# Kernel optimization log

Hardware: AMD Instinct MI355X
Metric: run time of the kernel (lower is better)

The kernel has to match this reference:

```python
import jax, jax.numpy as jnp
import numpy as np

N_NODES = 50000
N_EDGES = 1600000
HIDDEN = 1024
NUM_CLASSES = 64


def setup_inputs() -> dict:
    key = jax.random.key(0)
    k1, k2, k3 = jax.random.split(key, 3)
    x = jax.random.normal(k1, (N_NODES, HIDDEN), dtype=jnp.float32)
    edge_index = jax.random.randint(k2, (2, N_EDGES), 0, N_NODES, dtype=jnp.int64)
    # Glorot-style init for the GCNConv linear weight, zero bias (PyG defaults)
    W = jax.random.normal(k3, (HIDDEN, NUM_CLASSES), dtype=jnp.float32) / np.sqrt(HIDDEN)
    b = jnp.zeros((NUM_CLASSES,), dtype=jnp.float32)
    return {"x": x, "edge_index": edge_index, "W": W, "b": b}


def reference(x, edge_index, W, b):
    # GCNConv: add self-loops, symmetric deg^{-1/2} normalization,
    # linear transform, gather-scale-scatter aggregation, bias, then softmax.
    n = x.shape[0]
    loops = jnp.arange(n, dtype=edge_index.dtype)
    src = jnp.concatenate([edge_index[0], loops])  # [E+N]
    dst = jnp.concatenate([edge_index[1], loops])  # [E+N]

    ones = jnp.ones(dst.shape[0], dtype=x.dtype)
    deg = jax.ops.segment_sum(ones, dst, num_segments=n)  # in-degree incl. self-loop
    deg_inv_sqrt = jnp.where(deg > 0, jax.lax.rsqrt(deg), 0.0)
    norm = deg_inv_sqrt[src] * deg_inv_sqrt[dst]  # [E+N]

    h = x @ W  # [N, C] dense GEMM (transform before propagate)
    msgs = h[src] * norm[:, None]  # gather + scale
    out = jax.ops.segment_sum(msgs, dst, num_segments=n) + b  # scatter-add
    return jax.nn.softmax(out, axis=1)
```

## Files before the change

kernel.cpp:

```cpp
#include <hip/hip_runtime.h>
#include <hip/hip_bf16.h>
#include <hip/hip_fp16.h>
#include <math.h>

#define HIDDEN 1024
#define NCLS 64
#define NB2 784
#define BCAP2 2560
#define CHUNK 4096
#define SMEM_BYTES 33280

typedef __attribute__((ext_vector_type(8))) short short8;
typedef __attribute__((ext_vector_type(4))) float f32x4;
typedef __attribute__((ext_vector_type(8))) _Float16 half8;

__device__ __forceinline__ short f2bf(float f) {
    __hip_bfloat16 b = __float2bfloat16(f);
    return __builtin_bit_cast(short, b);
}
__device__ __forceinline__ float bf2f(short s) {
    unsigned u = ((unsigned)(unsigned short)s) << 16;
    return __builtin_bit_cast(float, u);
}

__device__ __forceinline__ void async_copy16(void* lds, const void* g) {
    __builtin_amdgcn_global_load_lds(
        (const __attribute__((address_space(1))) unsigned int*)g,
        (__attribute__((address_space(3))) unsigned int*)lds, 16, 0, 0);
}

__global__ void wprep_kernel(const float* __restrict__ W,
                             short* __restrict__ wt_hi, short* __restrict__ wt_lo) {
    int idx = blockIdx.x * 256 + threadIdx.x;
    int c = idx >> 10;
    int k = idx & 1023;
    float f = W[(size_t)k * NCLS + c];
    short hb = f2bf(f);
    wt_hi[idx] = hb;
    wt_lo[idx] = f2bf(f - bf2f(hb));
}

__device__ void bucket_body(char* smem, const int* __restrict__ ei,
                            unsigned* __restrict__ pairs2, int* __restrict__ bcnt2,
                            int E, int bid) {
    int* hist  = (int*)smem;
    int* offs  = hist + 1024;
    int* cur   = offs + 1024;
    int* gbase = cur + 1024;
    unsigned* stage = (unsigned*)(gbase + 1024);
    int* nz = (int*)(stage + CHUNK);
    int* wsum = nz + 1;

    const int tid = threadIdx.x;
    const int base = bid * CHUNK;
    const int cnt_c = min(CHUNK, E - base);

    if (tid == 0) *nz = 0;
    #pragma unroll
    for (int j = 0; j < 4; ++j) { hist[tid + 256 * j] = 0; cur[tid + 256 * j] = 0; }
    __syncthreads();

    int found = 0;
    for (int j = tid; j < 1024; j += 256) {
        int e = base + j;
        if (e < E) found |= (ei[2 * e + 1] != 0);
    }
    if (found) atomicOr(nz, 1);
    __syncthreads();
    const int is64 = (*nz == 0);

    unsigned pr[16];
    #pragma unroll
    for (int j = 0; j < 16; ++j) {
        int e = base + j * 256 + tid;
        unsigned p = 0xFFFFFFFFu;
        if (e < E) {
            int s = is64 ? ei[2 * e] : ei[e];
            int d = is64 ? ei[2 * (E + e)] : ei[E + e];
            p = (unsigned)s | ((unsigned)d << 16);
            atomicAdd(&hist[d >> 6], 1);
        }
        pr[j] = p;
    }
    __syncthreads();

    const int b0 = 4 * tid;
    int h0 = hist[b0], h1 = hist[b0 + 1], h2 = hist[b0 + 2], h3 = hist[b0 + 3];
    int S = h0 + h1 + h2 + h3;
    int incl = S;
    #pragma unroll
    for (int d = 1; d < 64; d <<= 1) {
        int t2 = __shfl_up(incl, d);
        if ((tid & 63) >= d) incl += t2;
    }
    if ((tid & 63) == 63) wsum[tid >> 6] = incl;
    __syncthreads();
    int pre = 0;
    #pragma unroll
    for (int w = 0; w < 4; ++w)
        if (w < (tid >> 6)) pre += wsum[w];
    int ex = pre + incl - S;
    offs[b0] = ex;
    offs[b0 + 1] = ex + h0;
    offs[b0 + 2] = ex + h0 + h1;
    offs[b0 + 3] = ex + h0 + h1 + h2;
    if (h0 > 0) gbase[b0] = atomicAdd(&bcnt2[b0], h0);
    if (h1 > 0) gbase[b0 + 1] = atomicAdd(&bcnt2[b0 + 1], h1);
    if (h2 > 0) gbase[b0 + 2] = atomicAdd(&bcnt2[b0 + 2], h2);
    if (h3 > 0) gbase[b0 + 3] = atomicAdd(&bcnt2[b0 + 3], h3);
    __syncthreads();

    #pragma unroll
    for (int j = 0; j < 16; ++j) {
        unsigned p = pr[j];
        if (p != 0xFFFFFFFFu) {
            int b = (int)(p >> 22);
            int pos = offs[b] + atomicAdd(&cur[b], 1);
            stage[pos] = p;
        }
    }
    __syncthreads();
    for (int i = tid; i < cnt_c; i += 256) {
        unsigned p = stage[i];
        int b = (int)(p >> 22);
        pairs2[(size_t)b * BCAP2 + gbase[b] + (i - offs[b])] = p;
    }
}

__device__ void gemm_body(char* smem, const float* __restrict__ x,
                          const short* __restrict__ wt_hi, const short* __restrict__ wt_lo,
                          _Float16* __restrict__ h16, int M, int bid) {
    char* As = smem;
    char* Bh = smem + 16 * 1040;
    char* Bl = smem + 24 * 1040;

    const int tid = threadIdx.x;
    const int wave = tid >> 6;
    const int lane = tid & 63;
    const int l15 = lane & 15, l4 = lane >> 4;
    const int row0 = bid * 64;

    const float* agp[4];
    #pragma unroll
    for (int i = 0; i < 4; ++i) {
        int rg = row0 + (wave * 4 + i) * 4 + (lane >> 4);
        if (rg > M - 1) rg = M - 1;
        int g = (lane & 15) ^ (((lane >> 4) & 3) << 2);
        agp[i] = x + (size_t)rg * HIDDEN + g * 4;
    }
    const short* bhp[2];
    const short* blp[2];
    #pragma unroll
    for (int i = 0; i < 2; ++i) {
        int c = (wave * 2 + i) * 8 + (lane >> 3);
        int g = (lane & 7) ^ ((lane >> 3) & 7);
        bhp[i] = wt_hi + (size_t)c * HIDDEN + g * 8;
        blp[i] = wt_lo + (size_t)c * HIDDEN + g * 8;
    }

    f32x4 acc[4];
    #pragma unroll
    for (int nf = 0; nf < 4; ++nf) acc[nf] = (f32x4){0.f, 0.f, 0.f, 0.f};

    const int rt = wave * 16 + l15;
    const int r3 = rt & 3;
    char* arow = As + (rt >> 2) * 1040 + r3 * 256;

    for (int k0 = 0; k0 < HIDDEN; k0 += 64) {
        #pragma unroll
        for (int i = 0; i < 4; ++i)
            async_copy16(As + (wave * 4 + i) * 1040, agp[i] + k0);
        #pragma unroll
        for (int i = 0; i < 2; ++i) {
            async_copy16(Bh + (wave * 2 + i) * 1040, bhp[i] + k0);
            async_copy16(Bl + (wave * 2 + i) * 1040, blp[i] + k0);
        }
        __syncthreads();

        #pragma unroll
        for (int kk = 0; kk < 2; ++kk) {
            int js = (kk * 8 + l4 * 2) ^ (r3 << 2);
            f32x4 af0 = *reinterpret_cast<const f32x4*>(arow + js * 16);
            f32x4 af1 = *reinterpret_cast<const f32x4*>(arow + js * 16 + 16);
            short8 ah, al;
            #pragma unroll
            for (int j = 0; j < 4; ++j) {
                short hb = f2bf(af0[j]);
                ah[j] = hb;
                al[j] = f2bf(af0[j] - bf2f(hb));
                short hb2 = f2bf(af1[j]);
                ah[j + 4] = hb2;
                al[j + 4] = f2bf(af1[j] - bf2f(hb2));
            }
            #pragma unroll
            for (int nf = 0; nf < 4; ++nf) {
                int c = l15 + 16 * nf;
                int jb = (kk * 4 + l4) ^ (c & 7);
                size_t boff = (size_t)(c >> 3) * 1040 + (c & 7) * 128 + jb * 16;
                short8 bh = *reinterpret_cast<const short8*>(Bh + boff);
                short8 bl = *reinterpret_cast<const short8*>(Bl + boff);
                acc[nf] = __builtin_amdgcn_mfma_f32_16x16x32_bf16(ah, bh, acc[nf], 0, 0, 0);
                acc[nf] = __builtin_amdgcn_mfma_f32_16x16x32_bf16(al, bh, acc[nf], 0, 0, 0);
                acc[nf] = __builtin_amdgcn_mfma_f32_16x16x32_bf16(ah, bl, acc[nf], 0, 0, 0);
            }
        }
        __syncthreads();
    }

    #pragma unroll
    for (int j = 0; j < 4; ++j) {
        int r = row0 + wave * 16 + l4 * 4 + j;
        if (r < M) {
            #pragma unroll
            for (int nf = 0; nf < 4; ++nf) {
                h16[(size_t)r * NCLS + l15 + 16 * nf] = (_Float16)acc[nf][j];
            }
        }
    }
}

__global__ __launch_bounds__(256) void fat_kernel(const float* __restrict__ x,
                                                  const short* __restrict__ wt_hi,
                                                  const short* __restrict__ wt_lo,
                                                  _Float16* __restrict__ h16, int M,
                                                  const int* __restrict__ ei,
                                                  unsigned* __restrict__ pairs2,
                                                  int* __restrict__ bcnt2, int E,
                                                  int nGemmGrid, int nTiles) {
    __shared__ __align__(16) char smem[SMEM_BYTES];
    const int bid = blockIdx.x;
    if (bid < nGemmGrid) {
        for (int t = bid; t < nTiles; t += nGemmGrid)
            gemm_body(smem, x, wt_hi, wt_lo, h16, M, t);
    } else {
        bucket_body(smem, ei, pairs2, bcnt2, E, bid - nGemmGrid);
    }
}

__global__ __launch_bounds__(256) void degree_kernel(const unsigned* __restrict__ pairs2,
                                                     const int* __restrict__ bcnt2,
                                                     float* __restrict__ dis, int n) {
    __shared__ int hist[256];
    const int tid = threadIdx.x;
    hist[tid] = 0;
    __syncthreads();
    #pragma unroll
    for (int gg = 0; gg < 4; ++gg) {
        int g = blockIdx.x * 4 + gg;
        const int cb = bcnt2[g];
        const unsigned* bp = pairs2 + (size_t)g * BCAP2;
        for (int i = tid; i < cb; i += 256)
            atomicAdd(&hist[gg * 64 + ((bp[i] >> 16) & 63)], 1);
    }
    __syncthreads();
    int node = blockIdx.x * 256 + tid;
    if (node < n) dis[node] = rsqrtf((float)hist[tid] + 1.0f);
}

__global__ __launch_bounds__(256) void agg_kernel(const unsigned* __restrict__ pairs2,
                                                  const int* __restrict__ bcnt2,
                                                  const _Float16* __restrict__ h16,
                                                  const float* __restrict__ dis,
                                                  const float* __restrict__ bias,
                                                  float* __restrict__ out, int n) {
    __shared__ int hist[64];
    __shared__ int offs[64];
    __shared__ int cur[64];
    __shared__ unsigned short ssrc[BCAP2];
    __shared__ float swt[BCAP2];
    const int tid = threadIdx.x;
    const int grp = blockIdx.x;
    const int base_node = grp * 64;
    if (base_node >= n) return;
    if (tid < 64) { hist[tid] = 0; cur[tid] = 0; }
    __syncthreads();
    const int cb = bcnt2[grp];
    const unsigned* bp = pairs2 + (size_t)grp * BCAP2;
    for (int i = tid; i < cb; i += 256)
        atomicAdd(&hist[(bp[i] >> 16) & 63], 1);
    __syncthreads();
    if (tid == 0) {
        int r = 0;
        #pragma unroll
        for (int k = 0; k < 64; ++k) { offs[k] = r; r += hist[k]; }
    }
    __syncthreads();
    for (int i = tid; i < cb; i += 256) {
        unsigned p = bp[i];
        int ln = (p >> 16) & 63;
        int pos = offs[ln] + atomicAdd(&cur[ln], 1);
        int s = (int)(p & 0xFFFFu);
        ssrc[pos] = (unsigned short)s;
        swt[pos] = dis[s];
    }
    __syncthreads();

    const int wave = tid >> 6;
    const int lane = tid & 63;
    const int q = lane & 7;
    const int g = lane >> 3;
    float bv[8];
    #pragma unroll
    for (int c = 0; c < 8; ++c) bv[c] = bias[q * 8 + c];

    for (int t = 0; t < 16; ++t) {
        int ln = wave * 16 + t;
        int node = base_node + ln;
        if (node >= n) continue;
        int len = hist[ln];
        int e0 = offs[ln];
        float di = rsqrtf((float)len + 1.0f);

        half8 hs = *reinterpret_cast<const half8*>(h16 + (size_t)node * NCLS + q * 8);
        float selfw = (g == 0) ? di : 0.f;
        float a[8], a2[8];
        #pragma unroll
        for (int c = 0; c < 8; ++c) { a[c] = (float)hs[c] * selfw; a2[c] = 0.f; }

        for (int i = 0; i < len; i += 16) {
            int i1 = i + g;
            bool v1 = i1 < len;
            int s1 = v1 ? (int)ssrc[e0 + i1] : 0;
            float w1 = v1 ? swt[e0 + i1] : 0.f;
            half8 r1 = *reinterpret_cast<const half8*>(h16 + (size_t)s1 * NCLS + q * 8);
            if (i + 8 < len) {
                int i2 = i + 8 + g;
                bool v2 = i2 < len;
                int s2 = v2 ? (int)ssrc[e0 + i2] : 0;
                float w2 = v2 ? swt[e0 + i2] : 0.f;
                half8 r2 = *reinterpret_cast<const half8*>(h16 + (size_t)s2 * NCLS + q * 8);
                #pragma unroll
                for (int c = 0; c < 8; ++c) a2[c] += w2 * (float)r2[c];
            }
            #pragma unroll
            for (int c = 0; c < 8; ++c) a[c] += w1 * (float)r1[c];
        }
        #pragma unroll
        for (int c = 0; c < 8; ++c) {
            float s = a[c] + a2[c];
            s += __shfl_xor(s, 8);
            s += __shfl_xor(s, 16);
            s += __shfl_xor(s, 32);
            a[c] = s * di + bv[c];
        }
        float m = a[0];
        #pragma unroll
        for (int c = 1; c < 8; ++c) m = fmaxf(m, a[c]);
        #pragma unroll
        for (int d = 1; d < 8; d <<= 1) m = fmaxf(m, __shfl_xor(m, d));
        float ex[8], sum = 0.f;
        #pragma unroll
        for (int c = 0; c < 8; ++c) { ex[c] = __expf(a[c] - m); sum += ex[c]; }
        #pragma unroll
        for (int d = 1; d < 8; d <<= 1) sum += __shfl_xor(sum, d);
        float inv = 1.f / sum;
        if (g == 0) {
            f32x4 o0 = {ex[0] * inv, ex[1] * inv, ex[2] * inv, ex[3] * inv};
            f32x4 o1 = {ex[4] * inv, ex[5] * inv, ex[6] * inv, ex[7] * inv};
            *reinterpret_cast<f32x4*>(out + (size_t)node * NCLS + q * 8) = o0;
            *reinterpret_cast<f32x4*>(out + (size_t)node * NCLS + q * 8 + 4) = o1;
        }
    }
}

extern "C" void kernel_launch(void* const* d_in, const int* in_sizes, int n_in,
                              void* d_out, int out_size, void* d_ws, size_t ws_size,
                              hipStream_t stream) {
    const float* x    = (const float*)d_in[0];
    const int*   ei   = (const int*)d_in[1];
    const float* W    = (const float*)d_in[2];
    const float* bias = (const float*)d_in[3];
    float* out = (float*)d_out;

    const int n = in_sizes[0] / HIDDEN;
    const int E = in_sizes[1] / 2;

    char* ws = (char*)d_ws;
    size_t off = 0;
    auto alloc = [&](size_t bytes) -> void* {
        void* p = (void*)(ws + off);
        off = (off + bytes + 255) & ~((size_t)255);
        return p;
    };
    int*      bcnt2  = (int*)alloc((size_t)NB2 * 4);
    unsigned* pairs2 = (unsigned*)alloc((size_t)NB2 * BCAP2 * 4);
    float*    dis    = (float*)alloc((size_t)n * 4);
    _Float16* h16    = (_Float16*)alloc((size_t)n * NCLS * 2);
    short*    wt_hi  = (short*)alloc((size_t)NCLS * HIDDEN * 2);
    short*    wt_lo  = (short*)alloc((size_t)NCLS * HIDDEN * 2);
    (void)ws_size;

    hipMemsetAsync(bcnt2, 0, (size_t)NB2 * 4, stream);

    wprep_kernel<<<(NCLS * HIDDEN) / 256, 256, 0, stream>>>(W, wt_hi, wt_lo);

    const int nTiles = (n + 63) / 64;
    const int nGemmGrid = (nTiles + 1) / 2;
    const int nBucketBlocks = (E + CHUNK - 1) / CHUNK;
    fat_kernel<<<nGemmGrid + nBucketBlocks, 256, 0, stream>>>(
        x, wt_hi, wt_lo, h16, n, ei, pairs2, bcnt2, E, nGemmGrid, nTiles);

    const int nGroups = (n + 63) / 64;
    degree_kernel<<<(nGroups + 3) / 4, 256, 0, stream>>>(pairs2, bcnt2, dis, n);
    agg_kernel<<<nGroups, 256, 0, stream>>>(pairs2, bcnt2, h16, dis, bias, out, n);
}
```

Measured before the change: 146.0 us.

## Widen GEMM tile to 128 rows, split accumulators, remap tiles per XCD

The fused GEMM block now computes 128 rows instead of 64, so each B (weight hi/lo) fragment loaded from LDS is reused across two 16-row A fragments per wave. The three-term bf16 split product now accumulates into two independent accumulator chains to shorten MFMA dependency stalls. Block-to-tile mapping is permuted so consecutive tiles land on the same XCD. The cost is more LDS per block, which may lower occupancy, and more registers.

Result: faster. 139.6 us (-4.4%).

```diff
diff --git a/kernel.cpp b/kernel.cpp
--- a/kernel.cpp
+++ b/kernel.cpp
@@ -8,7 +8,7 @@
 #define NB2 784
 #define BCAP2 2560
 #define CHUNK 4096
-#define SMEM_BYTES 33280
+#define SMEM_BYTES 49920
 
 typedef __attribute__((ext_vector_type(8))) short short8;
 typedef __attribute__((ext_vector_type(4))) float f32x4;
@@ -131,19 +131,19 @@
                           const short* __restrict__ wt_hi, const short* __restrict__ wt_lo,
                           _Float16* __restrict__ h16, int M, int bid) {
     char* As = smem;
-    char* Bh = smem + 16 * 1040;
-    char* Bl = smem + 24 * 1040;
+    char* Bh = smem + 32 * 1040;
+    char* Bl = smem + 40 * 1040;
 
     const int tid = threadIdx.x;
     const int wave = tid >> 6;
     const int lane = tid & 63;
     const int l15 = lane & 15, l4 = lane >> 4;
-    const int row0 = bid * 64;
-
-    const float* agp[4];
-    #pragma unroll
-    for (int i = 0; i < 4; ++i) {
-        int rg = row0 + (wave * 4 + i) * 4 + (lane >> 4);
+    const int row0 = bid * 128;
+
+    const float* agp[8];
+    #pragma unroll
+    for (int i = 0; i < 8; ++i) {
+        int rg = row0 + (wave * 8 + i) * 4 + (lane >> 4);
         if (rg > M - 1) rg = M - 1;
         int g = (lane & 15) ^ (((lane >> 4) & 3) << 2);
         agp[i] = x + (size_t)rg * HIDDEN + g * 4;
@@ -158,18 +158,24 @@
         blp[i] = wt_lo + (size_t)c * HIDDEN + g * 8;
     }
 
-    f32x4 acc[4];
-    #pragma unroll
-    for (int nf = 0; nf < 4; ++nf) acc[nf] = (f32x4){0.f, 0.f, 0.f, 0.f};
-
-    const int rt = wave * 16 + l15;
+    f32x4 accP[2][4], accQ[2][4];
+    #pragma unroll
+    for (int f = 0; f < 2; ++f)
+        #pragma unroll
+        for (int nf = 0; nf < 4; ++nf) {
+            accP[f][nf] = (f32x4){0.f, 0.f, 0.f, 0.f};
+            accQ[f][nf] = (f32x4){0.f, 0.f, 0.f, 0.f};
+        }
+
+    const int rt = wave * 32 + l15;
     const int r3 = rt & 3;
-    char* arow = As + (rt >> 2) * 1040 + r3 * 256;
+    char* arow0 = As + (rt >> 2) * 1040 + r3 * 256;
+    char* arow1 = arow0 + 4 * 1040;
 
     for (int k0 = 0; k0 < HIDDEN; k0 += 64) {
         #pragma unroll
-        for (int i = 0; i < 4; ++i)
-            async_copy16(As + (wave * 4 + i) * 1040, agp[i] + k0);
+        for (int i = 0; i < 8; ++i)
+            async_copy16(As + (wave * 8 + i) * 1040, agp[i] + k0);
         #pragma unroll
         for (int i = 0; i < 2; ++i) {
             async_copy16(Bh + (wave * 2 + i) * 1040, bhp[i] + k0);
@@ -180,17 +186,18 @@
         #pragma unroll
         for (int kk = 0; kk < 2; ++kk) {
             int js = (kk * 8 + l4 * 2) ^ (r3 << 2);
-            f32x4 af0 = *reinterpret_cast<const f32x4*>(arow + js * 16);
-            f32x4 af1 = *reinterpret_cast<const f32x4*>(arow + js * 16 + 16);
-            short8 ah, al;
+            f32x4 a00 = *reinterpret_cast<const f32x4*>(arow0 + js * 16);
+            f32x4 a01 = *reinterpret_cast<const f32x4*>(arow0 + (js ^ 1) * 16);
+            f32x4 a10 = *reinterpret_cast<const f32x4*>(arow1 + js * 16);
+            f32x4 a11 = *reinterpret_cast<const f32x4*>(arow1 + (js ^ 1) * 16);
+            short8 ah0, al0, ah1, al1;
             #pragma unroll
             for (int j = 0; j < 4; ++j) {
-                short hb = f2bf(af0[j]);
-                ah[j] = hb;
-                al[j] = f2bf(af0[j] - bf2f(hb));
-                short hb2 = f2bf(af1[j]);
-                ah[j + 4] = hb2;
-                al[j + 4] = f2bf(af1[j] - bf2f(hb2));
+                short hb;
+                hb = f2bf(a00[j]); ah0[j] = hb; al0[j] = f2bf(a00[j] - bf2f(hb));
+                hb = f2bf(a01[j]); ah0[j + 4] = hb; al0[j + 4] = f2bf(a01[j] - bf2f(hb));
+                hb = f2bf(a10[j]); ah1[j] = hb; al1[j] = f2bf(a10[j] - bf2f(hb));
+                hb = f2bf(a11[j]); ah1[j + 4] = hb; al1[j + 4] = f2bf(a11[j] - bf2f(hb));
             }
             #pragma unroll
             for (int nf = 0; nf < 4; ++nf) {
@@ -199,21 +206,28 @@
                 size_t boff = (size_t)(c >> 3) * 1040 + (c & 7) * 128 + jb * 16;
                 short8 bh = *reinterpret_cast<const short8*>(Bh + boff);
                 short8 bl = *reinterpret_cast<const short8*>(Bl + boff);
-                acc[nf] = __builtin_amdgcn_mfma_f32_16x16x32_bf16(ah, bh, acc[nf], 0, 0, 0);
-                acc[nf] = __builtin_amdgcn_mfma_f32_16x16x32_bf16(al, bh, acc[nf], 0, 0, 0);
-                acc[nf] = __builtin_amdgcn_mfma_f32_16x16x32_bf16(ah, bl, acc[nf], 0, 0, 0);
+                accP[0][nf] = __builtin_amdgcn_mfma_f32_16x16x32_bf16(ah0, bh, accP[0][nf], 0, 0, 0);
+                accP[0][nf] = __builtin_amdgcn_mfma_f32_16x16x32_bf16(al0, bh, accP[0][nf], 0, 0, 0);
+                accQ[0][nf] = __builtin_amdgcn_mfma_f32_16x16x32_bf16(ah0, bl, accQ[0][nf], 0, 0, 0);
+                accP[1][nf] = __builtin_amdgcn_mfma_f32_16x16x32_bf16(ah1, bh, accP[1][nf], 0, 0, 0);
+                accP[1][nf] = __builtin_amdgcn_mfma_f32_16x16x32_bf16(al1, bh, accP[1][nf], 0, 0, 0);
+                accQ[1][nf] = __builtin_amdgcn_mfma_f32_16x16x32_bf16(ah1, bl, accQ[1][nf], 0, 0, 0);
             }
         }
         __syncthreads();
     }
 
     #pragma unroll
-    for (int j = 0; j < 4; ++j) {
-        int r = row0 + wave * 16 + l4 * 4 + j;
-        if (r < M) {
-            #pragma unroll
-            for (int nf = 0; nf < 4; ++nf) {
-                h16[(size_t)r * NCLS + l15 + 16 * nf] = (_Float16)acc[nf][j];
+    for (int f = 0; f < 2; ++f) {
+        #pragma unroll
+        for (int j = 0; j < 4; ++j) {
+            int r = row0 + wave * 32 + f * 16 + l4 * 4 + j;
+            if (r < M) {
+                #pragma unroll
+                for (int nf = 0; nf < 4; ++nf) {
+                    h16[(size_t)r * NCLS + l15 + 16 * nf] =
+                        (_Float16)(accP[f][nf][j] + accQ[f][nf][j]);
+                }
             }
         }
     }
@@ -226,14 +240,16 @@
                                                   const int* __restrict__ ei,
                                                   unsigned* __restrict__ pairs2,
                                                   int* __restrict__ bcnt2, int E,
-                                                  int nGemmGrid, int nTiles) {
+                                                  int nGemm) {
     __shared__ __align__(16) char smem[SMEM_BYTES];
     const int bid = blockIdx.x;
-    if (bid < nGemmGrid) {
-        for (int t = bid; t < nTiles; t += nGemmGrid)
-            gemm_body(smem, x, wt_hi, wt_lo, h16, M, t);
+    if (bid < nGemm) {
+        const int q = nGemm >> 3, r = nGemm & 7;
+        int xcd = bid & 7, i = bid >> 3;
+        int t = (xcd < r ? xcd * (q + 1) : r * (q + 1) + (xcd - r) * q) + i;
+        gemm_body(smem, x, wt_hi, wt_lo, h16, M, t);
     } else {
-        bucket_body(smem, ei, pairs2, bcnt2, E, bid - nGemmGrid);
+        bucket_body(smem, ei, pairs2, bcnt2, E, bid - nGemm);
     }
 }
 
@@ -394,11 +410,10 @@
 
     wprep_kernel<<<(NCLS * HIDDEN) / 256, 256, 0, stream>>>(W, wt_hi, wt_lo);
 
-    const int nTiles = (n + 63) / 64;
-    const int nGemmGrid = (nTiles + 1) / 2;
+    const int nGemm = (n + 127) / 128;
     const int nBucketBlocks = (E + CHUNK - 1) / CHUNK;
-    fat_kernel<<<nGemmGrid + nBucketBlocks, 256, 0, stream>>>(
-        x, wt_hi, wt_lo, h16, n, ei, pairs2, bcnt2, E, nGemmGrid, nTiles);
+    fat_kernel<<<nGemm + nBucketBlocks, 256, 0, stream>>>(
+        x, wt_hi, wt_lo, h16, n, ei, pairs2, bcnt2, E, nGemm);
 
     const int nGroups = (n + 63) / 64;
     degree_kernel<<<(nGroups + 3) / 4, 256, 0, stream>>>(pairs2, bcnt2, dis, n);
```
